# Kernel optimization log

Hardware: AMD Instinct MI355X
Metric: run time of the kernel (lower is better)

The kernel has to match this reference:

```python
import jax, jax.numpy as jnp
import numpy as np

D_MODEL = 1024
NUM_HEADS = 16
DEPTH = D_MODEL // NUM_HEADS
B, S = 2, 2048


def setup_inputs() -> dict:
    key = jax.random.key(0)
    ks = jax.random.split(key, 8)
    scale = 1.0 / np.sqrt(D_MODEL)
    return {
        "v": jax.random.normal(ks[0], (B, S, D_MODEL), jnp.float32),
        "k": jax.random.normal(ks[1], (B, S, D_MODEL), jnp.float32),
        "q": jax.random.normal(ks[2], (B, S, D_MODEL), jnp.float32),
        "mask": jnp.zeros((B, 1, 1, S), jnp.float32),
        "wq": jax.random.normal(ks[3], (D_MODEL, D_MODEL), jnp.float32) * scale,
        "wk": jax.random.normal(ks[4], (D_MODEL, D_MODEL), jnp.float32) * scale,
        "wv": jax.random.normal(ks[5], (D_MODEL, D_MODEL), jnp.float32) * scale,
        "wo": jax.random.normal(ks[6], (D_MODEL, D_MODEL), jnp.float32) * scale,
        "bq": jnp.zeros((D_MODEL,), jnp.float32),
        "bk": jnp.zeros((D_MODEL,), jnp.float32),
        "bv": jnp.zeros((D_MODEL,), jnp.float32),
        "bo": jnp.zeros((D_MODEL,), jnp.float32),
    }


def _split_heads(x):
    # [B, S, d_model] -> [B, H, S, depth]
    b, s, _ = x.shape
    return x.reshape(b, s, NUM_HEADS, DEPTH).transpose(0, 2, 1, 3)


def reference(v, k, q, mask, wq, wk, wv, wo, bq, bk, bv, bo):
    qh = _split_heads(q @ wq + bq)
    kh = _split_heads(k @ wk + bk)
    vh = _split_heads(v @ wv + bv)
    # scores: [B, H, Sq, Sk]
    scores = jnp.einsum("bhqd,bhkd->bhqk", qh, kh) / jnp.sqrt(
        jnp.asarray(DEPTH, jnp.float32))
    scores = scores + mask * -1e9
    attn = jax.nn.softmax(scores, axis=-1)
    out = jnp.einsum("bhqk,bhkd->bhqd", attn, vh)  # [B, H, Sq, depth]
    out = out.transpose(0, 2, 1, 3).reshape(q.shape[0], -1, D_MODEL)
    out = out @ wo + bo
    return out, attn
```

## Files before the change

kernel.cpp:

```cpp
#include <hip/hip_runtime.h>

#define S_LEN 2048
#define DM 1024
#define NH 16
#define DH 64

typedef __attribute__((ext_vector_type(8))) short short8;
typedef __attribute__((ext_vector_type(4))) float f32x4;
typedef __attribute__((ext_vector_type(16))) float f32x16;
typedef unsigned short u16;
typedef unsigned int u32;

__device__ __forceinline__ u16 f2b(float f){
  union { float f; u32 u; } v; v.f = f;
  return (u16)((v.u + 0x7fffu + ((v.u >> 16) & 1u)) >> 16);
}
__device__ __forceinline__ float b2f(u16 h){
  union { u32 u; float f; } v; v.u = ((u32)h) << 16; return v.f;
}

__device__ __forceinline__ f32x4 mfma16(short8 a, short8 b, f32x4 c){
  return __builtin_amdgcn_mfma_f32_16x16x32_bf16(a, b, c, 0, 0, 0);
}
__device__ __forceinline__ f32x16 mfma32(short8 a, short8 b, f32x16 c){
  return __builtin_amdgcn_mfma_f32_32x32x16_bf16(a, b, c, 0, 0, 0);
}

#define SC2 0.18033688f

#if defined(__has_builtin)
#  if __has_builtin(__builtin_amdgcn_exp2f)
#    define EXP2(x) __builtin_amdgcn_exp2f(x)
#  else
#    define EXP2(x) __expf((x) * 0.6931472f)
#  endif
#else
#  define EXP2(x) __expf((x) * 0.6931472f)
#endif

template<int R, int NT>
__device__ __forceinline__ void stage_tile(const u16* src, int ld, u16* lds){
  const int t = threadIdx.x;
  #pragma unroll
  for (int it = 0; it < R*8/NT; ++it){
    int idx = it*NT + t;
    int row = idx >> 3;
    int ch  = (idx & 7) ^ (row & 7);
    const u16* g = src + row*ld + ch*8;
    u16* l = lds + (it*NT + (t & ~63))*8;
    __builtin_amdgcn_global_load_lds((const __attribute__((address_space(1))) void*)g,
                                     (__attribute__((address_space(3))) void*)l, 16, 0, 0);
  }
}

__device__ __forceinline__ short8 frag_ld(const u16* tile, int row, int ch){
  int off = (row*128 + ch*16) ^ ((row & 7) << 4);
  return *(const short8*)((const char*)tile + off);
}

__global__ __launch_bounds__(256) void k_cast(
    const float* __restrict__ q, const float* __restrict__ k, const float* __restrict__ v,
    u16* __restrict__ qb, u16* __restrict__ kb, u16* __restrict__ vb)
{
  int z = blockIdx.z;
  const float* src = (z==0)?q:(z==1)?k:v;
  u16* dst = (z==0)?qb:(z==1)?kb:vb;
  long i = ((long)blockIdx.x*256 + threadIdx.x)*8;
  f32x4 a = *(const f32x4*)(src + i);
  f32x4 b = *(const f32x4*)(src + i + 4);
  short8 o;
  #pragma unroll
  for (int j = 0; j < 4; ++j){ o[j] = (short)f2b(a[j]); o[4+j] = (short)f2b(b[j]); }
  *(short8*)(dst + i) = o;
}

__global__ __launch_bounds__(256) void k_maskb(const float* __restrict__ mask,
                                               float* __restrict__ maskb)
{
  int i = blockIdx.x*256 + threadIdx.x;
  maskb[i] = -1.44269504e9f * mask[i];
}

__global__ __launch_bounds__(256) void k_transpose(
    const float* __restrict__ wq, const float* __restrict__ wk,
    const float* __restrict__ wv, const float* __restrict__ wo,
    u16* __restrict__ oq, u16* __restrict__ ok, u16* __restrict__ ov, u16* __restrict__ oo)
{
  int z = blockIdx.z;
  const float* W = (z==0)?wq:(z==1)?wk:(z==2)?wv:wo;
  u16* O = (z==0)?oq:(z==1)?ok:(z==2)?ov:oo;
  int k0 = blockIdx.x*64, n0 = blockIdx.y*64;
  __shared__ float tl[64][65];
  int t = threadIdx.x;
  #pragma unroll
  for (int i = 0; i < 16; ++i){
    int idx = i*256 + t;
    int row = idx >> 6, col = idx & 63;
    tl[row][col] = W[(long)(k0+row)*DM + n0 + col];
  }
  __syncthreads();
  #pragma unroll
  for (int i = 0; i < 16; ++i){
    int idx = i*256 + t;
    int n = idx >> 6, kk = idx & 63;
    O[(long)(n0+n)*DM + k0 + kk] = f2b(tl[kk][n]);
  }
}

__device__ __forceinline__ void gemm_body(const u16* __restrict__ X, const u16* __restrict__ WT,
    const float* __restrict__ bias, u16* __restrict__ dst16, float* __restrict__ dst32,
    int layout, int m0, int n0, u16* At, u16* Bt)
{
  const int t = threadIdx.x, lane = t & 63, w = t >> 6;
  const int wr = (w >> 1) * 64, wc = (w & 1) * 64;
  const int li = lane & 15, lg = lane >> 4;
  const f32x4 zero = {0.f, 0.f, 0.f, 0.f};
  f32x4 acc[4][4];
  #pragma unroll
  for (int m = 0; m < 4; ++m)
    #pragma unroll
    for (int n = 0; n < 4; ++n) acc[m][n] = zero;

  for (int kt = 0; kt < DM/64; ++kt){
    stage_tile<128,256>(X  + (long)m0*DM + kt*64, DM, At);
    stage_tile<128,256>(WT + (long)n0*DM + kt*64, DM, Bt);
    __syncthreads();
    #pragma unroll
    for (int ks = 0; ks < 2; ++ks){
      int ch = ks*4 + lg;
      short8 a[4], b[4];
      #pragma unroll
      for (int m = 0; m < 4; ++m) a[m] = frag_ld(At, wr + m*16 + li, ch);
      #pragma unroll
      for (int n = 0; n < 4; ++n) b[n] = frag_ld(Bt, wc + n*16 + li, ch);
      #pragma unroll
      for (int m = 0; m < 4; ++m)
        #pragma unroll
        for (int n = 0; n < 4; ++n) acc[m][n] = mfma16(a[m], b[n], acc[m][n]);
    }
    __syncthreads();
  }

  if (layout == 1){
    f32x4 bm[4];
    #pragma unroll
    for (int m = 0; m < 4; ++m) bm[m] = *(const f32x4*)(bias + m0 + wr + m*16 + lg*4);
    #pragma unroll
    for (int m = 0; m < 4; ++m)
      #pragma unroll
      for (int n = 0; n < 4; ++n)
        #pragma unroll
        for (int r = 0; r < 4; ++r){
          int gm = m0 + wr + m*16 + lg*4 + r;
          int gc = n0 + wc + n*16 + li;
          int hh = gm >> 6, dd = gm & 63, bb = gc >> 11, ss = gc & (S_LEN-1);
          dst16[(((long)(bb*NH + hh))*DH + dd)*S_LEN + ss] = f2b(acc[m][n][r] + bm[m][r]);
        }
  } else {
    float bv4[4];
    #pragma unroll
    for (int n = 0; n < 4; ++n) bv4[n] = bias[n0 + wc + n*16 + li];
    #pragma unroll
    for (int m = 0; m < 4; ++m)
      #pragma unroll
      for (int n = 0; n < 4; ++n)
        #pragma unroll
        for (int r = 0; r < 4; ++r){
          int gm = m0 + wr + m*16 + lg*4 + r;
          int gc = n0 + wc + n*16 + li;
          float val = acc[m][n][r] + bv4[n];
          if (layout == 0){
            int bb = gm >> 11, ss = gm & (S_LEN-1), hh = gc >> 6, dd = gc & 63;
            dst16[(((long)(bb*NH + hh))*S_LEN + ss)*DH + dd] = f2b(val);
          } else {
            dst32[(long)gm*DM + gc] = val;
          }
        }
  }
}

__global__ __launch_bounds__(256) void k_gemm_qkv(
    const u16* __restrict__ qb, const u16* __restrict__ kb, const u16* __restrict__ vb,
    const u16* __restrict__ wtq, const u16* __restrict__ wtk, const u16* __restrict__ wtv,
    const float* __restrict__ bq, const float* __restrict__ bk, const float* __restrict__ bv,
    u16* __restrict__ Qw, u16* __restrict__ Kw, u16* __restrict__ VTw)
{
  __shared__ u16 At[128*64], Bt[128*64];
  int bid = blockIdx.x;
  int xcd = bid & 7, j = bid >> 3;
  int z = j >> 5, tt = j & 31;
  int mi = xcd*4 + (tt >> 3), n = tt & 7;
  if (z == 2){
    gemm_body(wtv, vb, bv, VTw, nullptr, 1, n*128, mi*128, At, Bt);
  } else {
    const u16* X  = (z==0)?qb:kb;
    const u16* WT = (z==0)?wtq:wtk;
    const float* B = (z==0)?bq:bk;
    u16* dst = (z==0)?Qw:Kw;
    gemm_body(X, WT, B, dst, nullptr, 0, mi*128, n*128, At, Bt);
  }
}

__global__ __launch_bounds__(256) void k_gemm_out(
    const u16* __restrict__ ctx, const u16* __restrict__ wto,
    const float* __restrict__ bo, float* __restrict__ out)
{
  __shared__ u16 At[128*64], Bt[128*64];
  int bid = blockIdx.x;
  int xcd = bid & 7, tt = bid >> 3;
  int mi = xcd*4 + (tt >> 3), n = tt & 7;
  gemm_body(ctx, wto, bo, nullptr, out, 2, mi*128, n*128, At, Bt);
}

__global__ __launch_bounds__(128) void k_attn1(const u16* __restrict__ Q,
    const u16* __restrict__ K, const float* __restrict__ maskb,
    float* __restrict__ lp0, float* __restrict__ lp1)
{
  __shared__ u16 Kt[2][64*64];
  const int t = threadIdx.x, lane = t & 63, w = t >> 6;
  const int lq = lane & 31, hi = lane >> 5;
  const int bid = blockIdx.x;
  const int xcd = bid & 7, j = bid >> 3;
  const int kh = j & 1, jj = j >> 1;
  const int bh = xcd + 8*(jj & 3);
  const int q0 = (jj >> 2) * 64;
  const int b = bh >> 4;
  const int k0 = kh * (S_LEN/2);
  const u16* Qb = Q + ((long)bh*S_LEN + q0 + w*32 + lq)*DH;
  short8 qa[4];
  #pragma unroll
  for (int ds = 0; ds < 4; ++ds) qa[ds] = *(const short8*)(Qb + ds*16 + hi*8);
  const float* mb_g = maskb + b*S_LEN + k0;
  const u16* Kb = K + ((long)bh*S_LEN + k0)*DH;

  float lsum = 0.f;
  stage_tile<64,128>(Kb, DH, Kt[0]);
  __syncthreads();
  for (int tt = 0; tt < S_LEN/128; ++tt){
    const u16* cur = Kt[tt & 1];
    if (tt + 1 < S_LEN/128)
      stage_tile<64,128>(Kb + (long)(tt+1)*64*DH, DH, Kt[(tt+1) & 1]);
    #pragma unroll
    for (int kt = 0; kt < 2; ++kt){
      f32x16 acc = {};
      __builtin_amdgcn_s_setprio(1);
      #pragma unroll
      for (int ds = 0; ds < 4; ++ds)
        acc = mfma32(frag_ld(cur, kt*32 + lq, ds*2 + hi), qa[ds], acc);
      __builtin_amdgcn_s_setprio(0);
      #pragma unroll
      for (int rg = 0; rg < 4; ++rg){
        f32x4 mb = *(const f32x4*)(mb_g + tt*64 + kt*32 + rg*8 + hi*4);
        #pragma unroll
        for (int jj2 = 0; jj2 < 4; ++jj2)
          lsum += EXP2(acc[rg*4+jj2]*SC2 + mb[jj2]);
      }
    }
    __syncthreads();
  }
  lsum += __shfl_xor(lsum, 32);
  if (hi == 0){
    float* lp = kh ? lp1 : lp0;
    lp[bh*S_LEN + q0 + w*32 + lq] = lsum;
  }
}

__global__ __launch_bounds__(256) void k_attn2(const u16* __restrict__ Q,
    const u16* __restrict__ K, const u16* __restrict__ VT,
    const float* __restrict__ maskb, const float* __restrict__ lp0,
    const float* __restrict__ lp1, float* __restrict__ attn, u16* __restrict__ ctx)
{
  __shared__ u16 Kt[2][64*64], Vt[2][64*64], Pt[128*64];
  const int t = threadIdx.x, lane = t & 63, w = t >> 6;
  const int lq = lane & 31, hi = lane >> 5;
  const int bid = blockIdx.x;
  const int xcd = bid & 7, j = bid >> 3;
  const int bh = xcd + 8*(j & 3);
  const int q0 = (j >> 2) * 128;
  const int b = bh >> 4;
  const u16* Qb = Q + ((long)bh*S_LEN + q0 + w*32 + lq)*DH;
  short8 qa[4];
  #pragma unroll
  for (int ds = 0; ds < 4; ++ds) qa[ds] = *(const short8*)(Qb + ds*16 + hi*8);
  const float* mb_g = maskb + b*S_LEN;
  const long lbase = (long)bh*S_LEN + q0 + w*32;

  float rlw[8];
  #pragma unroll
  for (int i = 0; i < 8; ++i){
    int qq = i*4 + (lane >> 4);
    rlw[i] = 1.f / (lp0[lbase + qq] + lp1[lbase + qq]);
  }

  f32x16 cacc[2] = {};
  const int prow = w*32 + lq;
  const int pswz = (prow & 7) << 4;

  stage_tile<64,256>(K  + (long)bh*S_LEN*DH, DH, Kt[0]);
  stage_tile<64,256>(VT + (long)bh*DH*S_LEN, S_LEN, Vt[0]);
  __syncthreads();
  for (int tt = 0; tt < S_LEN/64; ++tt){
    const int cur = tt & 1;
    if (tt + 1 < S_LEN/64){
      stage_tile<64,256>(K  + ((long)bh*S_LEN + (tt+1)*64)*DH, DH, Kt[cur^1]);
      stage_tile<64,256>(VT + (long)bh*DH*S_LEN + (tt+1)*64, S_LEN, Vt[cur^1]);
    }
    #pragma unroll
    for (int kt = 0; kt < 2; ++kt){
      f32x16 acc = {};
      __builtin_amdgcn_s_setprio(1);
      #pragma unroll
      for (int ds = 0; ds < 4; ++ds)
        acc = mfma32(frag_ld(Kt[cur], kt*32 + lq, ds*2 + hi), qa[ds], acc);
      __builtin_amdgcn_s_setprio(0);
      #pragma unroll
      for (int rg = 0; rg < 4; ++rg){
        f32x4 mb = *(const f32x4*)(mb_g + tt*64 + kt*32 + rg*8 + hi*4);
        float p0 = EXP2(acc[rg*4+0]*SC2 + mb[0]);
        float p1 = EXP2(acc[rg*4+1]*SC2 + mb[1]);
        float p2 = EXP2(acc[rg*4+2]*SC2 + mb[2]);
        float p3 = EXP2(acc[rg*4+3]*SC2 + mb[3]);
        uint2 pu;
        pu.x = (u32)f2b(p0) | ((u32)f2b(p1) << 16);
        pu.y = (u32)f2b(p2) | ((u32)f2b(p3) << 16);
        int off = (prow*128 + (kt*32 + rg*8 + hi*4)*2) ^ pswz;
        *(uint2*)((char*)Pt + off) = pu;
      }
    }
    #pragma unroll
    for (int i = 0; i < 8; ++i){
      int rr = i*4 + (lane >> 4);
      int ch8 = lane & 15;
      int roff = ((w*32 + rr)*128 + ch8*8) ^ ((rr & 7) << 4);
      uint2 pr = *(const uint2*)((const char*)Pt + roff);
      f32x4 av;
      av[0] = b2f((u16)(pr.x & 0xffffu)) * rlw[i];
      av[1] = b2f((u16)(pr.x >> 16))     * rlw[i];
      av[2] = b2f((u16)(pr.y & 0xffffu)) * rlw[i];
      av[3] = b2f((u16)(pr.y >> 16))     * rlw[i];
      *(f32x4*)(attn + ((long)bh*S_LEN + q0 + w*32 + rr)*S_LEN + tt*64 + ch8*4) = av;
    }
    short8 pa[4];
    #pragma unroll
    for (int ks = 0; ks < 4; ++ks) pa[ks] = frag_ld(Pt, prow, ks*2 + hi);
    __builtin_amdgcn_s_setprio(1);
    #pragma unroll
    for (int dh = 0; dh < 2; ++dh)
      #pragma unroll
      for (int ks = 0; ks < 4; ++ks)
        cacc[dh] = mfma32(pa[ks], frag_ld(Vt[cur], dh*32 + lq, ks*2 + hi), cacc[dh]);
    __builtin_amdgcn_s_setprio(0);
    asm volatile("s_waitcnt vmcnt(8)" ::: "memory");
    __builtin_amdgcn_sched_barrier(0);
    __builtin_amdgcn_s_barrier();
  }

  int bb = bh >> 4, hh = bh & 15;
  #pragma unroll
  for (int r = 0; r < 16; ++r){
    int qrow = (r & 3) + 8*(r >> 2) + 4*hi;
    float rle = 1.f / (lp0[lbase + qrow] + lp1[lbase + qrow]);
    #pragma unroll
    for (int dh = 0; dh < 2; ++dh){
      float val = cacc[dh][r] * rle;
      ctx[((long)bb*S_LEN + q0 + w*32 + qrow)*DM + hh*DH + dh*32 + lq] = f2b(val);
    }
  }
}

extern "C" void kernel_launch(void* const* d_in, const int* in_sizes, int n_in,
                              void* d_out, int out_size, void* d_ws, size_t ws_size,
                              hipStream_t stream)
{
  const float* v_in = (const float*)d_in[0];
  const float* k_in = (const float*)d_in[1];
  const float* q_in = (const float*)d_in[2];
  const float* mask = (const float*)d_in[3];
  const float* wq = (const float*)d_in[4];
  const float* wk = (const float*)d_in[5];
  const float* wv = (const float*)d_in[6];
  const float* wo = (const float*)d_in[7];
  const float* bq = (const float*)d_in[8];
  const float* bk = (const float*)d_in[9];
  const float* bv = (const float*)d_in[10];
  const float* bo = (const float*)d_in[11];

  float* out  = (float*)d_out;
  float* attn = out + (long)2*S_LEN*DM;

  char* ws = (char*)d_ws;
  const long MW = 1024*1024;
  u16*  wtq = (u16*)(ws);
  u16*  wtk = (u16*)(ws + 2*MW);
  u16*  wtv = (u16*)(ws + 4*MW);
  u16*  wto = (u16*)(ws + 6*MW);
  u16*  qb  = (u16*)(ws + 8*MW);
  u16*  kb  = (u16*)(ws + 17*MW);
  u16*  vb  = (u16*)(ws + 26*MW);
  u16*  Qw  = (u16*)(ws + 35*MW);
  u16*  Kw  = (u16*)(ws + 44*MW);
  u16*  VTw = (u16*)(ws + 53*MW);
  u16*  ctx = (u16*)(ws + 8*MW);
  float* lp0   = (float*)(ws + 62*MW);
  float* lp1   = (float*)(ws + 62*MW + 262144);
  float* maskb = (float*)(ws + 63*MW);

  k_cast<<<dim3(2048,1,3), 256, 0, stream>>>(q_in, k_in, v_in, qb, kb, vb);
  k_maskb<<<16, 256, 0, stream>>>(mask, maskb);
  k_transpose<<<dim3(16,16,4), 256, 0, stream>>>(wq,wk,wv,wo, wtq,wtk,wtv,wto);
  k_gemm_qkv<<<768, 256, 0, stream>>>(qb,kb,vb, wtq,wtk,wtv, bq,bk,bv, Qw,Kw,VTw);
  k_attn1<<<2048, 128, 0, stream>>>(Qw, Kw, maskb, lp0, lp1);
  k_attn2<<<512, 256, 0, stream>>>(Qw, Kw, VTw, maskb, lp0, lp1, attn, ctx);
  k_gemm_out<<<256, 256, 0, stream>>>(ctx, wto, bo, out);
}
```

Before: 289.0 us.

## Merge preprocessing kernels into one launch and widen attn1 blocks to four waves

The separate cast, mask-scale and weight-transpose kernels are folded into a single k_pre launch that branches on block index, which removes two kernel launches and their gaps. k_attn1 moves from 128 to 256 threads per block, so each block covers 128 queries and shares each staged K tile across four waves instead of two. The attn1 grid is halved to match. This cuts K reloads and launch overhead, at the cost of fewer, larger blocks and a __syncthreads inside a divergent branch of k_pre (safe only because the condition is uniform per block).

After: 287.5 us. No clear change (-0.5%).

```diff
diff --git a/kernel.cpp b/kernel.cpp
--- a/kernel.cpp
+++ b/kernel.cpp
@@ -58,52 +58,49 @@
   return *(const short8*)((const char*)tile + off);
 }
 
-__global__ __launch_bounds__(256) void k_cast(
+__global__ __launch_bounds__(256) void k_pre(
     const float* __restrict__ q, const float* __restrict__ k, const float* __restrict__ v,
-    u16* __restrict__ qb, u16* __restrict__ kb, u16* __restrict__ vb)
-{
-  int z = blockIdx.z;
-  const float* src = (z==0)?q:(z==1)?k:v;
-  u16* dst = (z==0)?qb:(z==1)?kb:vb;
-  long i = ((long)blockIdx.x*256 + threadIdx.x)*8;
-  f32x4 a = *(const f32x4*)(src + i);
-  f32x4 b = *(const f32x4*)(src + i + 4);
-  short8 o;
-  #pragma unroll
-  for (int j = 0; j < 4; ++j){ o[j] = (short)f2b(a[j]); o[4+j] = (short)f2b(b[j]); }
-  *(short8*)(dst + i) = o;
-}
-
-__global__ __launch_bounds__(256) void k_maskb(const float* __restrict__ mask,
-                                               float* __restrict__ maskb)
-{
-  int i = blockIdx.x*256 + threadIdx.x;
-  maskb[i] = -1.44269504e9f * mask[i];
-}
-
-__global__ __launch_bounds__(256) void k_transpose(
+    u16* __restrict__ qb, u16* __restrict__ kb, u16* __restrict__ vb,
     const float* __restrict__ wq, const float* __restrict__ wk,
     const float* __restrict__ wv, const float* __restrict__ wo,
-    u16* __restrict__ oq, u16* __restrict__ ok, u16* __restrict__ ov, u16* __restrict__ oo)
-{
-  int z = blockIdx.z;
-  const float* W = (z==0)?wq:(z==1)?wk:(z==2)?wv:wo;
-  u16* O = (z==0)?oq:(z==1)?ok:(z==2)?ov:oo;
-  int k0 = blockIdx.x*64, n0 = blockIdx.y*64;
+    u16* __restrict__ oq, u16* __restrict__ ok, u16* __restrict__ ov, u16* __restrict__ oo,
+    const float* __restrict__ mask, float* __restrict__ maskb)
+{
   __shared__ float tl[64][65];
-  int t = threadIdx.x;
-  #pragma unroll
-  for (int i = 0; i < 16; ++i){
-    int idx = i*256 + t;
-    int row = idx >> 6, col = idx & 63;
-    tl[row][col] = W[(long)(k0+row)*DM + n0 + col];
-  }
-  __syncthreads();
-  #pragma unroll
-  for (int i = 0; i < 16; ++i){
-    int idx = i*256 + t;
-    int n = idx >> 6, kk = idx & 63;
-    O[(long)(n0+n)*DM + k0 + kk] = f2b(tl[kk][n]);
+  const int bid = blockIdx.x, t = threadIdx.x;
+  if (bid < 6144){
+    int z = bid >> 11, xi = bid & 2047;
+    const float* src = (z==0)?q:(z==1)?k:v;
+    u16* dst = (z==0)?qb:(z==1)?kb:vb;
+    long i = ((long)xi*256 + t)*8;
+    f32x4 a = *(const f32x4*)(src + i);
+    f32x4 b = *(const f32x4*)(src + i + 4);
+    short8 o;
+    #pragma unroll
+    for (int j = 0; j < 4; ++j){ o[j] = (short)f2b(a[j]); o[4+j] = (short)f2b(b[j]); }
+    *(short8*)(dst + i) = o;
+  } else if (bid < 7168){
+    int idx = bid - 6144;
+    int z = idx >> 8, rem = idx & 255;
+    const float* W = (z==0)?wq:(z==1)?wk:(z==2)?wv:wo;
+    u16* O = (z==0)?oq:(z==1)?ok:(z==2)?ov:oo;
+    int k0 = (rem >> 4)*64, n0 = (rem & 15)*64;
+    #pragma unroll
+    for (int i = 0; i < 16; ++i){
+      int idx2 = i*256 + t;
+      int row = idx2 >> 6, col = idx2 & 63;
+      tl[row][col] = W[(long)(k0+row)*DM + n0 + col];
+    }
+    __syncthreads();
+    #pragma unroll
+    for (int i = 0; i < 16; ++i){
+      int idx2 = i*256 + t;
+      int n = idx2 >> 6, kk = idx2 & 63;
+      O[(long)(n0+n)*DM + k0 + kk] = f2b(tl[kk][n]);
+    }
+  } else {
+    int i = (bid - 7168)*256 + t;
+    maskb[i] = -1.44269504e9f * mask[i];
   }
 }
 
@@ -212,7 +209,7 @@
   gemm_body(ctx, wto, bo, nullptr, out, 2, mi*128, n*128, At, Bt);
 }
 
-__global__ __launch_bounds__(128) void k_attn1(const u16* __restrict__ Q,
+__global__ __launch_bounds__(256) void k_attn1(const u16* __restrict__ Q,
     const u16* __restrict__ K, const float* __restrict__ maskb,
     float* __restrict__ lp0, float* __restrict__ lp1)
 {
@@ -223,7 +220,7 @@
   const int xcd = bid & 7, j = bid >> 3;
   const int kh = j & 1, jj = j >> 1;
   const int bh = xcd + 8*(jj & 3);
-  const int q0 = (jj >> 2) * 64;
+  const int q0 = (jj >> 2) * 128;
   const int b = bh >> 4;
   const int k0 = kh * (S_LEN/2);
   const u16* Qb = Q + ((long)bh*S_LEN + q0 + w*32 + lq)*DH;
@@ -234,12 +231,12 @@
   const u16* Kb = K + ((long)bh*S_LEN + k0)*DH;
 
   float lsum = 0.f;
-  stage_tile<64,128>(Kb, DH, Kt[0]);
+  stage_tile<64,256>(Kb, DH, Kt[0]);
   __syncthreads();
   for (int tt = 0; tt < S_LEN/128; ++tt){
     const u16* cur = Kt[tt & 1];
     if (tt + 1 < S_LEN/128)
-      stage_tile<64,128>(Kb + (long)(tt+1)*64*DH, DH, Kt[(tt+1) & 1]);
+      stage_tile<64,256>(Kb + (long)(tt+1)*64*DH, DH, Kt[(tt+1) & 1]);
     #pragma unroll
     for (int kt = 0; kt < 2; ++kt){
       f32x16 acc = {};
@@ -405,11 +402,11 @@
   float* lp1   = (float*)(ws + 62*MW + 262144);
   float* maskb = (float*)(ws + 63*MW);
 
-  k_cast<<<dim3(2048,1,3), 256, 0, stream>>>(q_in, k_in, v_in, qb, kb, vb);
-  k_maskb<<<16, 256, 0, stream>>>(mask, maskb);
-  k_transpose<<<dim3(16,16,4), 256, 0, stream>>>(wq,wk,wv,wo, wtq,wtk,wtv,wto);
+  k_pre<<<7184, 256, 0, stream>>>(q_in, k_in, v_in, qb, kb, vb,
+                                  wq, wk, wv, wo, wtq, wtk, wtv, wto,
+                                  mask, maskb);
   k_gemm_qkv<<<768, 256, 0, stream>>>(qb,kb,vb, wtq,wtk,wtv, bq,bk,bv, Qw,Kw,VTw);
-  k_attn1<<<2048, 128, 0, stream>>>(Qw, Kw, maskb, lp0, lp1);
+  k_attn1<<<1024, 256, 0, stream>>>(Qw, Kw, maskb, lp0, lp1);
   k_attn2<<<512, 256, 0, stream>>>(Qw, Kw, VTw, maskb, lp0, lp1, attn, ctx);
   k_gemm_out<<<256, 256, 0, stream>>>(ctx, wto, bo, out);
 }
```
